# Kernel tuning notes

Measured on AMD Instinct MI355X. Metric: run time of the kernel, lower is better.

## Reference

```python
import jax, jax.numpy as jnp
import numpy as np
import math

B, LQ, LK, D = 16, 2048, 2048, 64

def setup_inputs() -> dict:
    key = jax.random.key(0)
    kq, kk, kv, kn = jax.random.split(key, 4)
    q = jax.random.normal(kq, (B, LQ, D), dtype=jnp.float32)
    k = jax.random.normal(kk, (B, LK, D), dtype=jnp.float32)
    v = jax.random.normal(kv, (B, LK, D), dtype=jnp.float32)
    # valid lengths in [1, LK] so no row is fully masked
    valid_num = jax.random.randint(kn, (B,), 1, LK + 1, dtype=jnp.int32)
    return {"q": q, "k": k, "v": v, "valid_num": valid_num}

def reference(q, k, v, valid_num):
    d = q.shape[-1]
    # [B, LQ, LK] scores
    scores = jnp.einsum('bqd,bkd->bqk', q, k) / math.sqrt(d)
    # 1D valid_num -> same key mask for every query row (matches repeat_interleave)
    key_pos = jnp.arange(k.shape[1], dtype=valid_num.dtype)  # [LK]
    mask = key_pos[None, None, :] < valid_num[:, None, None]  # [B,1,LK] -> broadcast
    scores = jnp.where(mask, scores, -jnp.inf)
    attn = jax.nn.softmax(scores, axis=-1)
    # dropout p=0.0 -> identity (eval/deterministic reference)
    return jnp.einsum('bqk,bkd->bqd', attn, v)
```

## Files before the change

### kernel.cpp

```cpp
#include <hip/hip_runtime.h>


namespace {

constexpr int NB  = 16;
constexpr int SLQ = 2048;
constexpr int SLK = 2048;
constexpr int DH  = 64;
constexpr int KB  = 64;
constexpr int QB  = 128;

typedef _Float16 half8  __attribute__((ext_vector_type(8)));
typedef _Float16 half4  __attribute__((ext_vector_type(4)));
typedef _Float16 half2t __attribute__((ext_vector_type(2)));
typedef float    f32x4  __attribute__((ext_vector_type(4)));

__device__ inline half2t pkrtz(float a, float b) {
    return __builtin_bit_cast(half2t, __builtin_amdgcn_cvt_pkrtz(a, b));
}

typedef const __attribute__((address_space(1))) void* gas1_t;
typedef __attribute__((address_space(3))) void* las3_t;
__device__ __forceinline__ void gld16(const void* g, void* l) {
    __builtin_amdgcn_global_load_lds((gas1_t)g, (las3_t)l, 16, 0, 0);
}

__global__ __launch_bounds__(256)
void prepass(const float* __restrict__ kg, const float* __restrict__ vg,
             const int* __restrict__ vn,
             _Float16* __restrict__ kws, _Float16* __restrict__ vws)
{
    __shared__ _Float16 VT[DH][72];
    const int t  = threadIdx.x;
    const int b  = blockIdx.x >> 5;
    const int kt = blockIdx.x & 31;
    if (kt * KB >= vn[b]) return;
    const size_t tileH = ((size_t)(b << 5) + kt) * 4096;

    {
        const float* kp = kg + ((size_t)b * SLK + (size_t)kt * KB) * DH + t * 16;
        f32x4 a0 = ((const f32x4*)kp)[0], a1 = ((const f32x4*)kp)[1];
        f32x4 a2 = ((const f32x4*)kp)[2], a3 = ((const f32x4*)kp)[3];
        union { half2t h2[4]; uint4 u; } o0, o1;
        o0.h2[0] = pkrtz(a0[0], a0[1]); o0.h2[1] = pkrtz(a0[2], a0[3]);
        o0.h2[2] = pkrtz(a1[0], a1[1]); o0.h2[3] = pkrtz(a1[2], a1[3]);
        o1.h2[0] = pkrtz(a2[0], a2[1]); o1.h2[1] = pkrtz(a2[2], a2[3]);
        o1.h2[2] = pkrtz(a3[0], a3[1]); o1.h2[3] = pkrtz(a3[2], a3[3]);
#pragma unroll
        for (int j = 0; j < 2; ++j) {
            const int n = 2 * t + j;
            const int rr = n >> 3, c = n & 7;
            const int dst = rr * 8 + (c ^ (rr & 7));
            *(uint4*)(kws + tileH + (size_t)dst * 8) = j ? o1.u : o0.u;
        }
    }
    {
        const int kr = t >> 2, d0 = (t & 3) * 16;
        const float* vp = vg + ((size_t)b * SLK + (size_t)kt * KB + kr) * DH + d0;
        f32x4 a0 = ((const f32x4*)vp)[0], a1 = ((const f32x4*)vp)[1];
        f32x4 a2 = ((const f32x4*)vp)[2], a3 = ((const f32x4*)vp)[3];
#pragma unroll
        for (int i = 0; i < 4; ++i) {
            VT[d0 + i][kr]      = (_Float16)a0[i];
            VT[d0 + 4 + i][kr]  = (_Float16)a1[i];
            VT[d0 + 8 + i][kr]  = (_Float16)a2[i];
            VT[d0 + 12 + i][kr] = (_Float16)a3[i];
        }
    }
    __syncthreads();
#pragma unroll
    for (int j = 0; j < 2; ++j) {
        const int n = 2 * t + j;
        const int d = n >> 3, c = n & 7;
        const int rsw = (d & 7) << 3;
        const int pA = 32 * (c >> 2) + 8 * ((2 * c) & 3) + 4 * ((c >> 1) & 1);
        const int pB = 32 * (c >> 2) + 8 * ((2 * c + 1) & 3) + 4 * ((c >> 1) & 1);
        half4 hA = *(const half4*)&VT[d][c * 8];
        half4 hB = *(const half4*)&VT[d][c * 8 + 4];
        *(half4*)(vws + tileH + (size_t)d * 64 + (pA ^ rsw)) = hA;
        *(half4*)(vws + tileH + (size_t)d * 64 + (pB ^ rsw)) = hB;
    }
}

__global__ __launch_bounds__(256)
void attn_fwd(const float* __restrict__ qg, const _Float16* __restrict__ k16,
              const _Float16* __restrict__ v16, const int* __restrict__ vn,
              _Float16* __restrict__ ws_acc, float* __restrict__ ws_ml,
              int nsplit, int tps)
{
    __shared__ __attribute__((aligned(16))) _Float16 KV[8192];

    const int t   = threadIdx.x;
    const int l   = t & 63;
    const int w   = t >> 6;
    const int q15 = l & 15;
    const int g   = l >> 4;
    const int swz = (q15 & 7) << 3;

    const int bid = blockIdx.x;
    int b, qt, s;
    if (nsplit == 4) {
        const int k2 = bid >> 8;
        s  = k2;
        b  = (((bid >> 4) & 15) + k2) & 15;
        qt = bid & 15;
    } else {
        qt = bid >> 4;
        b  = ((bid & 15) + qt) & 15;
        s  = 0;
    }

    const int valid = vn[b];
    const int nkt   = (valid + KB - 1) / KB;
    const int kt0   = s * tps;
    if (kt0 >= nkt) return;
    const int kt1   = min(nkt, kt0 + tps);

    const int qrow0 = qt * QB + w * 16 + q15;
    const int qrow1 = qrow0 + 64;

    const float QS = 0.18033688011112042f;

    half8 qf[2][2];
#pragma unroll
    for (int qi = 0; qi < 2; ++qi) {
        const float* qp = qg + ((size_t)b * SLQ + (qi ? qrow1 : qrow0)) * DH;
#pragma unroll
        for (int ss = 0; ss < 2; ++ss) {
            const int d0 = 8 * g + 32 * ss;
            f32x4 x = *(const f32x4*)(qp + d0);
            f32x4 y = *(const f32x4*)(qp + d0 + 4);
            half8 h;
#pragma unroll
            for (int i = 0; i < 4; ++i) {
                h[i]     = (_Float16)(x[i] * QS);
                h[i + 4] = (_Float16)(y[i] * QS);
            }
            qf[qi][ss] = h;
        }
    }

    f32x4 acc0[4], acc1[4];
#pragma unroll
    for (int i = 0; i < 4; ++i) { acc0[i] = f32x4{0.f,0.f,0.f,0.f}; acc1[i] = f32x4{0.f,0.f,0.f,0.f}; }
    float m0 = -1e30f, l0 = 0.f, m1 = -1e30f, l1 = 0.f;

    const char* kbase = (const char*)(k16 + (size_t)(b << 5) * 4096);
    const char* vbase = (const char*)(v16 + (size_t)(b << 5) * 4096);
    const int wchunk = w * 128;

#define STAGE(KT)                                                              \
    {                                                                          \
        const char* kp_ = kbase + (size_t)(KT) * 8192;                         \
        const char* vp_ = vbase + (size_t)(KT) * 8192;                         \
        char* kl_ = (char*)&KV[0];                                             \
        char* vl_ = (char*)&KV[4096];                                          \
        gld16(kp_ + (wchunk + l) * 16,       kl_ + wchunk * 16);               \
        gld16(kp_ + (wchunk + 64 + l) * 16,  kl_ + (wchunk + 64) * 16);        \
        gld16(vp_ + (wchunk + l) * 16,       vl_ + wchunk * 16);               \
        gld16(vp_ + (wchunk + 64 + l) * 16,  vl_ + (wchunk + 64) * 16);        \
    }

    auto softmax_pack = [&](f32x4 (&st)[4], float& m, float& lsum,
                            f32x4 (&acc)[4], half2t (&pk)[4][2]) {
        float x0 = fmaxf(fmaxf(st[0][0], st[0][1]), fmaxf(st[0][2], st[0][3]));
        float x1 = fmaxf(fmaxf(st[1][0], st[1][1]), fmaxf(st[1][2], st[1][3]));
        float x2 = fmaxf(fmaxf(st[2][0], st[2][1]), fmaxf(st[2][2], st[2][3]));
        float x3 = fmaxf(fmaxf(st[3][0], st[3][1]), fmaxf(st[3][2], st[3][3]));
        float tmax = fmaxf(fmaxf(x0, x1), fmaxf(x2, x3));
        tmax = fmaxf(tmax, __shfl_xor(tmax, 16));
        tmax = fmaxf(tmax, __shfl_xor(tmax, 32));
        if (!__all(tmax - m <= 12.0f)) {
            const float mn = fmaxf(m, tmax);
            const float sc = __builtin_amdgcn_exp2f(m - mn);
            lsum *= sc;
#pragma unroll
            for (int mt = 0; mt < 4; ++mt) acc[mt] *= sc;
            m = mn;
        }
        float p[4][4];
#pragma unroll
        for (int mt = 0; mt < 4; ++mt)
#pragma unroll
            for (int r = 0; r < 4; ++r)
                p[mt][r] = __builtin_amdgcn_exp2f(st[mt][r] - m);
        float s0 = (p[0][0] + p[0][1]) + (p[0][2] + p[0][3]);
        float s1 = (p[1][0] + p[1][1]) + (p[1][2] + p[1][3]);
        float s2 = (p[2][0] + p[2][1]) + (p[2][2] + p[2][3]);
        float s3 = (p[3][0] + p[3][1]) + (p[3][2] + p[3][3]);
        float ps = (s0 + s1) + (s2 + s3);
        ps += __shfl_xor(ps, 16);
        ps += __shfl_xor(ps, 32);
        lsum += ps;
#pragma unroll
        for (int mt = 0; mt < 4; ++mt)
#pragma unroll
            for (int rr = 0; rr < 2; ++rr)
                pk[mt][rr] = pkrtz(p[mt][2 * rr], p[mt][2 * rr + 1]);
    };

    for (int kt = kt0; kt < kt1; ++kt) {
        __syncthreads();
        STAGE(kt);
        __syncthreads();

        const _Float16* Kc = &KV[0];
        const _Float16* Vc = &KV[4096];

        f32x4 st0[4], st1[4];
        __builtin_amdgcn_s_setprio(1);
#pragma unroll
        for (int mt = 0; mt < 4; ++mt) {
            f32x4 c0 = f32x4{0.f,0.f,0.f,0.f}, c1 = f32x4{0.f,0.f,0.f,0.f};
#pragma unroll
            for (int ss = 0; ss < 2; ++ss) {
                half8 a = *(const half8*)&Kc[(16 * mt + q15) * 64 + ((8 * g + 32 * ss) ^ swz)];
                c0 = __builtin_amdgcn_mfma_f32_16x16x32_f16(a, qf[0][ss], c0, 0, 0, 0);
                c1 = __builtin_amdgcn_mfma_f32_16x16x32_f16(a, qf[1][ss], c1, 0, 0, 0);
            }
            st0[mt] = c0; st1[mt] = c1;
        }
        __builtin_amdgcn_s_setprio(0);

        const int krem = valid - kt * KB;
        if (krem < KB) {
#pragma unroll
            for (int mt = 0; mt < 4; ++mt)
#pragma unroll
                for (int r = 0; r < 4; ++r)
                    if (16 * mt + 4 * g + r >= krem) { st0[mt][r] = -1e30f; st1[mt][r] = -1e30f; }
        }

        half2t pk0[4][2], pk1[4][2];
        softmax_pack(st0, m0, l0, acc0, pk0);
        softmax_pack(st1, m1, l1, acc1, pk1);

        __builtin_amdgcn_s_setprio(1);
#pragma unroll
        for (int ss = 0; ss < 2; ++ss) {
            union { half2t h2[4]; half8 v; } bf0, bf1;
            bf0.h2[0] = pk0[2 * ss][0]; bf0.h2[1] = pk0[2 * ss][1];
            bf0.h2[2] = pk0[2 * ss + 1][0]; bf0.h2[3] = pk0[2 * ss + 1][1];
            bf1.h2[0] = pk1[2 * ss][0]; bf1.h2[1] = pk1[2 * ss][1];
            bf1.h2[2] = pk1[2 * ss + 1][0]; bf1.h2[3] = pk1[2 * ss + 1][1];
#pragma unroll
            for (int mt = 0; mt < 4; ++mt) {
                half8 af = *(const half8*)&Vc[(16 * mt + q15) * 64 + ((32 * ss + 8 * g) ^ swz)];
                acc0[mt] = __builtin_amdgcn_mfma_f32_16x16x32_f16(af, bf0.v, acc0[mt], 0, 0, 0);
                acc1[mt] = __builtin_amdgcn_mfma_f32_16x16x32_f16(af, bf1.v, acc1[mt], 0, 0, 0);
            }
        }
        __builtin_amdgcn_s_setprio(0);
    }
#undef STAGE

#pragma unroll
    for (int qi = 0; qi < 2; ++qi) {
        const float ll  = qi ? l1 : l0;
        const float mm  = qi ? m1 : m0;
        const float inv = 1.0f / ll;
        f32x4* ac = qi ? acc1 : acc0;
        const size_t row = (size_t)b * SLQ + (qi ? qrow1 : qrow0);
        _Float16* wp = ws_acc + ((size_t)s * NB * SLQ + row) * DH;
#pragma unroll
        for (int mt = 0; mt < 4; ++mt) {
            union { half2t h2[2]; uint2 u; } o;
            o.h2[0] = pkrtz(ac[mt][0] * inv, ac[mt][1] * inv);
            o.h2[1] = pkrtz(ac[mt][2] * inv, ac[mt][3] * inv);
            *(uint2*)(wp + 16 * mt + 4 * g) = o.u;
        }
        if (g == 0)
            *(float2*)(ws_ml + ((size_t)s * NB * SLQ + row) * 2) = make_float2(mm, ll);
    }
}

__global__ __launch_bounds__(256)
void attn_combine(const _Float16* __restrict__ ws_acc, const float* __restrict__ ws_ml,
                  const int* __restrict__ vn, float* __restrict__ og,
                  int nsplit, int tps)
{
    const int tid = blockIdx.x * 256 + threadIdx.x;
    const int row = tid >> 2;
    const int dq  = (tid & 3) << 4;
    const int b   = row >> 11;

    const int valid = vn[b];
    const int nkt   = (valid + KB - 1) / KB;
    const int nact  = min(nsplit, (nkt + tps - 1) / tps);

    float M = -1e30f;
    for (int s = 0; s < nact; ++s)
        M = fmaxf(M, ws_ml[((size_t)s * NB * SLQ + row) * 2]);

    float L = 0.f;
    f32x4 o[4];
#pragma unroll
    for (int i = 0; i < 4; ++i) o[i] = f32x4{0.f, 0.f, 0.f, 0.f};

    for (int s = 0; s < nact; ++s) {
        const float2 ml = *(const float2*)(ws_ml + ((size_t)s * NB * SLQ + row) * 2);
        const float wl = __builtin_amdgcn_exp2f(ml.x - M) * ml.y;
        L += wl;
        const _Float16* ap = ws_acc + ((size_t)s * NB * SLQ + row) * DH + dq;
        half8 h0 = ((const half8*)ap)[0];
        half8 h1 = ((const half8*)ap)[1];
#pragma unroll
        for (int r = 0; r < 4; ++r) {
            o[0][r] += wl * (float)h0[r];
            o[1][r] += wl * (float)h0[4 + r];
            o[2][r] += wl * (float)h1[r];
            o[3][r] += wl * (float)h1[4 + r];
        }
    }

    const float inv = 1.0f / L;
    float* op = og + (size_t)row * DH + dq;
#pragma unroll
    for (int i = 0; i < 4; ++i) {
        f32x4 r = o[i] * inv;
        *(f32x4*)(op + 4 * i) = r;
    }
}

}

extern "C" void kernel_launch(void* const* d_in, const int* in_sizes, int n_in,
                              void* d_out, int out_size, void* d_ws, size_t ws_size,
                              hipStream_t stream)
{
    const float* q    = (const float*)d_in[0];
    const float* k    = (const float*)d_in[1];
    const float* v    = (const float*)d_in[2];
    const int*   vnum = (const int*)d_in[3];
    float* out = (float*)d_out;

    const size_t k16H  = (size_t)NB * SLK * DH;
    const size_t v16H  = k16H;
    const size_t rowsH = (size_t)NB * SLQ;

    int nsplit = 4;
    {
        const size_t need4 = (k16H + v16H + (size_t)4 * rowsH * DH) * 2
                           + (size_t)4 * rowsH * 2 * 4;
        if (ws_size < need4) nsplit = 1;
    }
    const int tps = (nsplit == 4) ? 8 : 32;

    _Float16* k16    = (_Float16*)d_ws;
    _Float16* v16t   = k16 + k16H;
    _Float16* ws_acc = v16t + v16H;
    float*    ws_ml  = (float*)(ws_acc + (size_t)nsplit * rowsH * DH);

    prepass<<<dim3(NB * (SLK / KB)), dim3(256), 0, stream>>>(k, v, vnum, k16, v16t);

    dim3 gfwd(nsplit == 4 ? 1024 : 256);
    attn_fwd<<<gfwd, dim3(256), 0, stream>>>(q, k16, v16t, vnum, ws_acc, ws_ml,
                                             nsplit, tps);

    attn_combine<<<dim3((NB * SLQ * 4) / 256), dim3(256), 0, stream>>>(
        ws_acc, ws_ml, vnum, out, nsplit, tps);
}
```

Before: 45.53 us.

## Fuse split-K combine into attention kernel via atomic ticket last-block reduction

Removes the separate combine kernel. Each attention block that finishes a split takes an atomic ticket for its (batch, q-tile), and the last block to arrive merges the partial results into the output. When only one split is active, the block writes normalized fp32 output directly and skips the workspace round-trip. The ticket counters are zeroed in the prepass kernel. This saves a kernel launch and the extra pass over workspace memory, at the cost of fences, an atomic and an uneven tail of work on the last-arriving blocks.

```diff
diff --git a/kernel.cpp b/kernel.cpp
--- a/kernel.cpp
+++ b/kernel.cpp
@@ -28,10 +28,12 @@
 __global__ __launch_bounds__(256)
 void prepass(const float* __restrict__ kg, const float* __restrict__ vg,
              const int* __restrict__ vn,
-             _Float16* __restrict__ kws, _Float16* __restrict__ vws)
+             _Float16* __restrict__ kws, _Float16* __restrict__ vws,
+             int* __restrict__ tickets)
 {
     __shared__ _Float16 VT[DH][72];
     const int t  = threadIdx.x;
+    if (blockIdx.x == 0) tickets[t] = 0;
     const int b  = blockIdx.x >> 5;
     const int kt = blockIdx.x & 31;
     if (kt * KB >= vn[b]) return;
@@ -85,10 +87,12 @@
 __global__ __launch_bounds__(256)
 void attn_fwd(const float* __restrict__ qg, const _Float16* __restrict__ k16,
               const _Float16* __restrict__ v16, const int* __restrict__ vn,
+              float* __restrict__ og,
               _Float16* __restrict__ ws_acc, float* __restrict__ ws_ml,
-              int nsplit, int tps)
+              int* __restrict__ tickets, int nsplit, int tps)
 {
     __shared__ __attribute__((aligned(16))) _Float16 KV[8192];
+    __shared__ int isLast;
 
     const int t   = threadIdx.x;
     const int l   = t & 63;
@@ -115,6 +119,7 @@
     const int kt0   = s * tps;
     if (kt0 >= nkt) return;
     const int kt1   = min(nkt, kt0 + tps);
+    const int nact  = min(nsplit, (nkt + tps - 1) / tps);
 
     const int qrow0 = qt * QB + w * 16 + q15;
     const int qrow1 = qrow0 + 64;
@@ -254,6 +259,23 @@
     }
 #undef STAGE
 
+    if (nact == 1) {
+#pragma unroll
+        for (int qi = 0; qi < 2; ++qi) {
+            const float inv = 1.0f / (qi ? l1 : l0);
+            f32x4* ac = qi ? acc1 : acc0;
+            float* op = og + ((size_t)b * SLQ + (qi ? qrow1 : qrow0)) * DH;
+#pragma unroll
+            for (int mt = 0; mt < 4; ++mt) {
+                f32x4 o;
+#pragma unroll
+                for (int r = 0; r < 4; ++r) o[r] = ac[mt][r] * inv;
+                *(f32x4*)(op + 16 * mt + 4 * g) = o;
+            }
+        }
+        return;
+    }
+
 #pragma unroll
     for (int qi = 0; qi < 2; ++qi) {
         const float ll  = qi ? l1 : l0;
@@ -272,53 +294,60 @@
         if (g == 0)
             *(float2*)(ws_ml + ((size_t)s * NB * SLQ + row) * 2) = make_float2(mm, ll);
     }
-}
-
-__global__ __launch_bounds__(256)
-void attn_combine(const _Float16* __restrict__ ws_acc, const float* __restrict__ ws_ml,
-                  const int* __restrict__ vn, float* __restrict__ og,
-                  int nsplit, int tps)
-{
-    const int tid = blockIdx.x * 256 + threadIdx.x;
-    const int row = tid >> 2;
-    const int dq  = (tid & 3) << 4;
-    const int b   = row >> 11;
-
-    const int valid = vn[b];
-    const int nkt   = (valid + KB - 1) / KB;
-    const int nact  = min(nsplit, (nkt + tps - 1) / tps);
-
-    float M = -1e30f;
-    for (int s = 0; s < nact; ++s)
-        M = fmaxf(M, ws_ml[((size_t)s * NB * SLQ + row) * 2]);
-
-    float L = 0.f;
-    f32x4 o[4];
-#pragma unroll
-    for (int i = 0; i < 4; ++i) o[i] = f32x4{0.f, 0.f, 0.f, 0.f};
-
-    for (int s = 0; s < nact; ++s) {
-        const float2 ml = *(const float2*)(ws_ml + ((size_t)s * NB * SLQ + row) * 2);
-        const float wl = __builtin_amdgcn_exp2f(ml.x - M) * ml.y;
-        L += wl;
-        const _Float16* ap = ws_acc + ((size_t)s * NB * SLQ + row) * DH + dq;
-        half8 h0 = ((const half8*)ap)[0];
-        half8 h1 = ((const half8*)ap)[1];
-#pragma unroll
-        for (int r = 0; r < 4; ++r) {
-            o[0][r] += wl * (float)h0[r];
-            o[1][r] += wl * (float)h0[4 + r];
-            o[2][r] += wl * (float)h1[r];
-            o[3][r] += wl * (float)h1[4 + r];
-        }
-    }
-
-    const float inv = 1.0f / L;
-    float* op = og + (size_t)row * DH + dq;
-#pragma unroll
-    for (int i = 0; i < 4; ++i) {
-        f32x4 r = o[i] * inv;
-        *(f32x4*)(op + 4 * i) = r;
+
+    __threadfence();
+    if (t == 0) {
+        int old = __hip_atomic_fetch_add(&tickets[(b << 4) | qt], 1,
+                                         __ATOMIC_ACQ_REL, __HIP_MEMORY_SCOPE_AGENT);
+        isLast = (old == nact - 1) ? 1 : 0;
+    }
+    __syncthreads();
+    if (!isLast) return;
+    __threadfence();
+
+    {
+        const int r  = t >> 1;
+        const int dq = (t & 1) * 32;
+        const size_t row = (size_t)b * SLQ + (size_t)qt * QB + r;
+
+        float M = -1e30f;
+        for (int s2 = 0; s2 < nact; ++s2)
+            M = fmaxf(M, ws_ml[((size_t)s2 * NB * SLQ + row) * 2]);
+
+        float L = 0.f;
+        f32x4 o[8];
+#pragma unroll
+        for (int i = 0; i < 8; ++i) o[i] = f32x4{0.f, 0.f, 0.f, 0.f};
+
+        for (int s2 = 0; s2 < nact; ++s2) {
+            const float2 ml = *(const float2*)(ws_ml + ((size_t)s2 * NB * SLQ + row) * 2);
+            const float wl = __builtin_amdgcn_exp2f(ml.x - M) * ml.y;
+            L += wl;
+            const _Float16* ap = ws_acc + ((size_t)s2 * NB * SLQ + row) * DH + dq;
+            half8 h0 = ((const half8*)ap)[0];
+            half8 h1 = ((const half8*)ap)[1];
+            half8 h2 = ((const half8*)ap)[2];
+            half8 h3 = ((const half8*)ap)[3];
+#pragma unroll
+            for (int r2 = 0; r2 < 4; ++r2) {
+                o[0][r2] += wl * (float)h0[r2];
+                o[1][r2] += wl * (float)h0[4 + r2];
+                o[2][r2] += wl * (float)h1[r2];
+                o[3][r2] += wl * (float)h1[4 + r2];
+                o[4][r2] += wl * (float)h2[r2];
+                o[5][r2] += wl * (float)h2[4 + r2];
+                o[6][r2] += wl * (float)h3[r2];
+                o[7][r2] += wl * (float)h3[4 + r2];
+            }
+        }
+
+        const float inv = 1.0f / L;
+        float* op = og + row * DH + dq;
+#pragma unroll
+        for (int i = 0; i < 8; ++i) {
+            f32x4 v = o[i] * inv;
+            *(f32x4*)(op + 4 * i) = v;
+        }
     }
 }
 
@@ -335,28 +364,25 @@
     float* out = (float*)d_out;
 
     const size_t k16H  = (size_t)NB * SLK * DH;
-    const size_t v16H  = k16H;
     const size_t rowsH = (size_t)NB * SLQ;
+
+    int*      tickets = (int*)d_ws;
+    _Float16* k16     = (_Float16*)((char*)d_ws + 1024);
+    _Float16* v16t    = k16 + k16H;
+    _Float16* ws_acc  = v16t + k16H;
+    float*    ws_ml   = (float*)(ws_acc + (size_t)4 * rowsH * DH);
 
     int nsplit = 4;
     {
-        const size_t need4 = (k16H + v16H + (size_t)4 * rowsH * DH) * 2
-                           + (size_t)4 * rowsH * 2 * 4;
-        if (ws_size < need4) nsplit = 1;
+        const size_t need = 1024 + ((size_t)2 * k16H + (size_t)4 * rowsH * DH) * 2
+                          + (size_t)4 * rowsH * 2 * 4;
+        if (ws_size < need) nsplit = 1;
     }
     const int tps = (nsplit == 4) ? 8 : 32;
 
-    _Float16* k16    = (_Float16*)d_ws;
-    _Float16* v16t   = k16 + k16H;
-    _Float16* ws_acc = v16t + v16H;
-    float*    ws_ml  = (float*)(ws_acc + (size_t)nsplit * rowsH * DH);
-
-    prepass<<<dim3(NB * (SLK / KB)), dim3(256), 0, stream>>>(k, v, vnum, k16, v16t);
+    prepass<<<dim3(NB * (SLK / KB)), dim3(256), 0, stream>>>(k, v, vnum, k16, v16t, tickets);
 
     dim3 gfwd(nsplit == 4 ? 1024 : 256);
-    attn_fwd<<<gfwd, dim3(256), 0, stream>>>(q, k16, v16t, vnum, ws_acc, ws_ml,
-                                             nsplit, tps);
-
-    attn_combine<<<dim3((NB * SLQ * 4) / 256), dim3(256), 0, stream>>>(
-        ws_acc, ws_ml, vnum, out, nsplit, tps);
-}
+    attn_fwd<<<gfwd, dim3(256), 0, stream>>>(q, k16, v16t, vnum, out,
+                                             ws_acc, ws_ml, tickets, nsplit, tps);
+}
```

Result: slower. 146.3 us (+221.2%).

## Read K/V fragments directly from global memory and write output directly for single-split rows

Applied to the files above, without the earlier changes.

Removes the LDS staging of K and V tiles, along with its block-wide barriers and priority hints. Each lane now loads its MFMA fragments straight from global memory, and the prepass writes K/V in a fragment-friendly layout without XOR swizzling. The query-row mapping changes so each wave owns 32 contiguous rows. When a batch's valid length needs only one split, attn_fwd writes the normalized fp32 output itself and the combine kernel skips those rows. This trades LDS reuse across the four waves for fewer barriers, relying on L1/L2 to serve the repeated reads of each tile by every wave.

```diff
diff --git a/kernel.cpp b/kernel.cpp
--- a/kernel.cpp
+++ b/kernel.cpp
@@ -8,7 +8,6 @@
 constexpr int SLK = 2048;
 constexpr int DH  = 64;
 constexpr int KB  = 64;
-constexpr int QB  = 128;
 
 typedef _Float16 half8  __attribute__((ext_vector_type(8)));
 typedef _Float16 half4  __attribute__((ext_vector_type(4)));
@@ -17,12 +16,6 @@
 
 __device__ inline half2t pkrtz(float a, float b) {
     return __builtin_bit_cast(half2t, __builtin_amdgcn_cvt_pkrtz(a, b));
-}
-
-typedef const __attribute__((address_space(1))) void* gas1_t;
-typedef __attribute__((address_space(3))) void* las3_t;
-__device__ __forceinline__ void gld16(const void* g, void* l) {
-    __builtin_amdgcn_global_load_lds((gas1_t)g, (las3_t)l, 16, 0, 0);
 }
 
 __global__ __launch_bounds__(256)
@@ -41,18 +34,13 @@
         const float* kp = kg + ((size_t)b * SLK + (size_t)kt * KB) * DH + t * 16;
         f32x4 a0 = ((const f32x4*)kp)[0], a1 = ((const f32x4*)kp)[1];
         f32x4 a2 = ((const f32x4*)kp)[2], a3 = ((const f32x4*)kp)[3];
-        union { half2t h2[4]; uint4 u; } o0, o1;
-        o0.h2[0] = pkrtz(a0[0], a0[1]); o0.h2[1] = pkrtz(a0[2], a0[3]);
-        o0.h2[2] = pkrtz(a1[0], a1[1]); o0.h2[3] = pkrtz(a1[2], a1[3]);
-        o1.h2[0] = pkrtz(a2[0], a2[1]); o1.h2[1] = pkrtz(a2[2], a2[3]);
-        o1.h2[2] = pkrtz(a3[0], a3[1]); o1.h2[3] = pkrtz(a3[2], a3[3]);
-#pragma unroll
-        for (int j = 0; j < 2; ++j) {
-            const int n = 2 * t + j;
-            const int rr = n >> 3, c = n & 7;
-            const int dst = rr * 8 + (c ^ (rr & 7));
-            *(uint4*)(kws + tileH + (size_t)dst * 8) = j ? o1.u : o0.u;
-        }
+        union { half2t h2[8]; uint4 u[2]; } o;
+        o.h2[0] = pkrtz(a0[0], a0[1]); o.h2[1] = pkrtz(a0[2], a0[3]);
+        o.h2[2] = pkrtz(a1[0], a1[1]); o.h2[3] = pkrtz(a1[2], a1[3]);
+        o.h2[4] = pkrtz(a2[0], a2[1]); o.h2[5] = pkrtz(a2[2], a2[3]);
+        o.h2[6] = pkrtz(a3[0], a3[1]); o.h2[7] = pkrtz(a3[2], a3[3]);
+        uint4* dst = (uint4*)(kws + tileH + (size_t)t * 16);
+        dst[0] = o.u[0]; dst[1] = o.u[1];
     }
     {
         const int kr = t >> 2, d0 = (t & 3) * 16;
@@ -72,42 +60,38 @@
     for (int j = 0; j < 2; ++j) {
         const int n = 2 * t + j;
         const int d = n >> 3, c = n & 7;
-        const int rsw = (d & 7) << 3;
         const int pA = 32 * (c >> 2) + 8 * ((2 * c) & 3) + 4 * ((c >> 1) & 1);
         const int pB = 32 * (c >> 2) + 8 * ((2 * c + 1) & 3) + 4 * ((c >> 1) & 1);
         half4 hA = *(const half4*)&VT[d][c * 8];
         half4 hB = *(const half4*)&VT[d][c * 8 + 4];
-        *(half4*)(vws + tileH + (size_t)d * 64 + (pA ^ rsw)) = hA;
-        *(half4*)(vws + tileH + (size_t)d * 64 + (pB ^ rsw)) = hB;
+        *(half4*)(vws + tileH + (size_t)d * 64 + pA) = hA;
+        *(half4*)(vws + tileH + (size_t)d * 64 + pB) = hB;
     }
 }
 
 __global__ __launch_bounds__(256)
 void attn_fwd(const float* __restrict__ qg, const _Float16* __restrict__ k16,
               const _Float16* __restrict__ v16, const int* __restrict__ vn,
+              float* __restrict__ og,
               _Float16* __restrict__ ws_acc, float* __restrict__ ws_ml,
               int nsplit, int tps)
 {
-    __shared__ __attribute__((aligned(16))) _Float16 KV[8192];
-
     const int t   = threadIdx.x;
     const int l   = t & 63;
     const int w   = t >> 6;
     const int q15 = l & 15;
     const int g   = l >> 4;
-    const int swz = (q15 & 7) << 3;
 
     const int bid = blockIdx.x;
-    int b, qt, s;
+    int b, qg_, s;
     if (nsplit == 4) {
-        const int k2 = bid >> 8;
-        s  = k2;
-        b  = (((bid >> 4) & 15) + k2) & 15;
-        qt = bid & 15;
+        s   = bid >> 8;
+        b   = (((bid >> 4) & 15) + s) & 15;
+        qg_ = bid & 15;
     } else {
-        qt = bid >> 4;
-        b  = ((bid & 15) + qt) & 15;
-        s  = 0;
+        qg_ = bid >> 4;
+        b   = ((bid & 15) + qg_) & 15;
+        s   = 0;
     }
 
     const int valid = vn[b];
@@ -115,9 +99,10 @@
     const int kt0   = s * tps;
     if (kt0 >= nkt) return;
     const int kt1   = min(nkt, kt0 + tps);
-
-    const int qrow0 = qt * QB + w * 16 + q15;
-    const int qrow1 = qrow0 + 64;
+    const int nact  = min(nsplit, (nkt + tps - 1) / tps);
+
+    const int qrow0 = qg_ * 128 + w * 32 + q15;
+    const int qrow1 = qrow0 + 16;
 
     const float QS = 0.18033688011112042f;
 
@@ -145,21 +130,7 @@
     for (int i = 0; i < 4; ++i) { acc0[i] = f32x4{0.f,0.f,0.f,0.f}; acc1[i] = f32x4{0.f,0.f,0.f,0.f}; }
     float m0 = -1e30f, l0 = 0.f, m1 = -1e30f, l1 = 0.f;
 
-    const char* kbase = (const char*)(k16 + (size_t)(b << 5) * 4096);
-    const char* vbase = (const char*)(v16 + (size_t)(b << 5) * 4096);
-    const int wchunk = w * 128;
-
-#define STAGE(KT)                                                              \
-    {                                                                          \
-        const char* kp_ = kbase + (size_t)(KT) * 8192;                         \
-        const char* vp_ = vbase + (size_t)(KT) * 8192;                         \
-        char* kl_ = (char*)&KV[0];                                             \
-        char* vl_ = (char*)&KV[4096];                                          \
-        gld16(kp_ + (wchunk + l) * 16,       kl_ + wchunk * 16);               \
-        gld16(kp_ + (wchunk + 64 + l) * 16,  kl_ + (wchunk + 64) * 16);        \
-        gld16(vp_ + (wchunk + l) * 16,       vl_ + wchunk * 16);               \
-        gld16(vp_ + (wchunk + 64 + l) * 16,  vl_ + (wchunk + 64) * 16);        \
-    }
+    const int fro = q15 * 64 + 8 * g;
 
     auto softmax_pack = [&](f32x4 (&st)[4], float& m, float& lsum,
                             f32x4 (&acc)[4], half2t (&pk)[4][2]) {
@@ -200,27 +171,20 @@
     };
 
     for (int kt = kt0; kt < kt1; ++kt) {
-        __syncthreads();
-        STAGE(kt);
-        __syncthreads();
-
-        const _Float16* Kc = &KV[0];
-        const _Float16* Vc = &KV[4096];
+        const _Float16* ktile = k16 + ((size_t)(b << 5) + kt) * 4096 + fro;
+        const _Float16* vtile = v16 + ((size_t)(b << 5) + kt) * 4096 + fro;
 
         f32x4 st0[4], st1[4];
-        __builtin_amdgcn_s_setprio(1);
 #pragma unroll
         for (int mt = 0; mt < 4; ++mt) {
-            f32x4 c0 = f32x4{0.f,0.f,0.f,0.f}, c1 = f32x4{0.f,0.f,0.f,0.f};
-#pragma unroll
-            for (int ss = 0; ss < 2; ++ss) {
-                half8 a = *(const half8*)&Kc[(16 * mt + q15) * 64 + ((8 * g + 32 * ss) ^ swz)];
-                c0 = __builtin_amdgcn_mfma_f32_16x16x32_f16(a, qf[0][ss], c0, 0, 0, 0);
-                c1 = __builtin_amdgcn_mfma_f32_16x16x32_f16(a, qf[1][ss], c1, 0, 0, 0);
-            }
+            half8 a0 = *(const half8*)(ktile + mt * 1024);
+            half8 a1 = *(const half8*)(ktile + mt * 1024 + 32);
+            f32x4 c0 = __builtin_amdgcn_mfma_f32_16x16x32_f16(a0, qf[0][0], f32x4{0.f,0.f,0.f,0.f}, 0, 0, 0);
+            f32x4 c1 = __builtin_amdgcn_mfma_f32_16x16x32_f16(a0, qf[1][0], f32x4{0.f,0.f,0.f,0.f}, 0, 0, 0);
+            c0 = __builtin_amdgcn_mfma_f32_16x16x32_f16(a1, qf[0][1], c0, 0, 0, 0);
+            c1 = __builtin_amdgcn_mfma_f32_16x16x32_f16(a1, qf[1][1], c1, 0, 0, 0);
             st0[mt] = c0; st1[mt] = c1;
         }
-        __builtin_amdgcn_s_setprio(0);
 
         const int krem = valid - kt * KB;
         if (krem < KB) {
@@ -235,7 +199,6 @@
         softmax_pack(st0, m0, l0, acc0, pk0);
         softmax_pack(st1, m1, l1, acc1, pk1);
 
-        __builtin_amdgcn_s_setprio(1);
 #pragma unroll
         for (int ss = 0; ss < 2; ++ss) {
             union { half2t h2[4]; half8 v; } bf0, bf1;
@@ -245,14 +208,29 @@
             bf1.h2[2] = pk1[2 * ss + 1][0]; bf1.h2[3] = pk1[2 * ss + 1][1];
 #pragma unroll
             for (int mt = 0; mt < 4; ++mt) {
-                half8 af = *(const half8*)&Vc[(16 * mt + q15) * 64 + ((32 * ss + 8 * g) ^ swz)];
+                half8 af = *(const half8*)(vtile + mt * 1024 + 32 * ss);
                 acc0[mt] = __builtin_amdgcn_mfma_f32_16x16x32_f16(af, bf0.v, acc0[mt], 0, 0, 0);
                 acc1[mt] = __builtin_amdgcn_mfma_f32_16x16x32_f16(af, bf1.v, acc1[mt], 0, 0, 0);
             }
         }
-        __builtin_amdgcn_s_setprio(0);
-    }
-#undef STAGE
+    }
+
+    if (nact == 1) {
+#pragma unroll
+        for (int qi = 0; qi < 2; ++qi) {
+            const float inv = 1.0f / (qi ? l1 : l0);
+            f32x4* ac = qi ? acc1 : acc0;
+            float* op = og + ((size_t)b * SLQ + (qi ? qrow1 : qrow0)) * DH;
+#pragma unroll
+            for (int mt = 0; mt < 4; ++mt) {
+                f32x4 o;
+#pragma unroll
+                for (int r = 0; r < 4; ++r) o[r] = ac[mt][r] * inv;
+                *(f32x4*)(op + 16 * mt + 4 * g) = o;
+            }
+        }
+        return;
+    }
 
 #pragma unroll
     for (int qi = 0; qi < 2; ++qi) {
@@ -287,6 +265,7 @@
     const int valid = vn[b];
     const int nkt   = (valid + KB - 1) / KB;
     const int nact  = min(nsplit, (nkt + tps - 1) / tps);
+    if (nact <= 1) return;
 
     float M = -1e30f;
     for (int s = 0; s < nact; ++s)
@@ -335,27 +314,26 @@
     float* out = (float*)d_out;
 
     const size_t k16H  = (size_t)NB * SLK * DH;
-    const size_t v16H  = k16H;
     const size_t rowsH = (size_t)NB * SLQ;
+
+    _Float16* k16    = (_Float16*)d_ws;
+    _Float16* v16t   = k16 + k16H;
+    _Float16* ws_acc = v16t + k16H;
+    float*    ws_ml  = (float*)(ws_acc + (size_t)4 * rowsH * DH);
 
     int nsplit = 4;
     {
-        const size_t need4 = (k16H + v16H + (size_t)4 * rowsH * DH) * 2
-                           + (size_t)4 * rowsH * 2 * 4;
-        if (ws_size < need4) nsplit = 1;
+        const size_t need = ((size_t)2 * k16H + (size_t)4 * rowsH * DH) * 2
+                          + (size_t)4 * rowsH * 2 * 4;
+        if (ws_size < need) nsplit = 1;
     }
     const int tps = (nsplit == 4) ? 8 : 32;
 
-    _Float16* k16    = (_Float16*)d_ws;
-    _Float16* v16t   = k16 + k16H;
-    _Float16* ws_acc = v16t + v16H;
-    float*    ws_ml  = (float*)(ws_acc + (size_t)nsplit * rowsH * DH);
-
     prepass<<<dim3(NB * (SLK / KB)), dim3(256), 0, stream>>>(k, v, vnum, k16, v16t);
 
     dim3 gfwd(nsplit == 4 ? 1024 : 256);
-    attn_fwd<<<gfwd, dim3(256), 0, stream>>>(q, k16, v16t, vnum, ws_acc, ws_ml,
-                                             nsplit, tps);
+    attn_fwd<<<gfwd, dim3(256), 0, stream>>>(q, k16, v16t, vnum, out,
+                                             ws_acc, ws_ml, nsplit, tps);
 
     attn_combine<<<dim3((NB * SLQ * 4) / 256), dim3(256), 0, stream>>>(
         ws_acc, ws_ml, vnum, out, nsplit, tps);
```

Result: slower. 61.05 us (+34.1%).
